# Performance work log

Hardware: AMD Instinct MI355X
Metric: run time of the kernel (lower is better)

Reference implementation:

```python
import jax, jax.numpy as jnp
import numpy as np

B, S, D, H = 2, 2048, 1024, 16
HD = D // H  # head_dim = 64


def setup_inputs() -> dict:
    key = jax.random.key(0)
    ks = jax.random.split(key, 5)
    scale = 1.0 / np.sqrt(D)
    return {
        "x": jax.random.normal(ks[0], (B, S, D), jnp.float32),
        "Wq": jax.random.normal(ks[1], (D, D), jnp.float32) * scale,
        "Wk": jax.random.normal(ks[2], (D, D), jnp.float32) * scale,
        "Wv": jax.random.normal(ks[3], (D, D), jnp.float32) * scale,
        "Wo": jax.random.normal(ks[4], (D, D), jnp.float32) * scale,
        "bo": jnp.zeros((D,), jnp.float32),
    }


def reference(x, Wq, Wk, Wv, Wo, bo):
    b, s, d = x.shape
    # torch nn.Linear: y = x @ W.T  (W stored [d_out, d_in])
    q = (x @ Wq.T).reshape(b, s, H, HD).transpose(0, 2, 1, 3)  # [b,h,s,hd]
    k = (x @ Wk.T).reshape(b, s, H, HD).transpose(0, 2, 1, 3)
    v = (x @ Wv.T).reshape(b, s, H, HD).transpose(0, 2, 1, 3)
    scores = jnp.einsum("bhqd,bhkd->bhqk", q, k) / jnp.sqrt(jnp.float32(HD))
    causal = jnp.triu(jnp.ones((s, s), dtype=bool), k=1)
    scores = jnp.where(causal[None, None], -jnp.inf, scores)
    attn = jax.nn.softmax(scores, axis=-1)
    ctx = jnp.einsum("bhqk,bhkd->bhqd", attn, v)
    ctx = ctx.transpose(0, 2, 1, 3).reshape(b, s, d)
    return ctx @ Wo.T + bo
```

## Files before the change

### kernel.cpp

```cpp
#include <hip/hip_runtime.h>

#define B_  2
#define S_  2048
#define D_  1024
#define H_  16
#define HD_ 64
#define M_  4096

typedef __attribute__((ext_vector_type(8))) short  short8;
typedef __attribute__((ext_vector_type(4))) float  floatx4;

__device__ __forceinline__ unsigned short f2bf(float f) {
  unsigned int u = __float_as_uint(f);
  u = (u + 0x7fffu + ((u >> 16) & 1u)) >> 16;
  return (unsigned short)u;
}

__device__ __forceinline__ void gl_lds16(const short* g, short* l) {
  __builtin_amdgcn_global_load_lds(
      (const __attribute__((address_space(1))) unsigned int*)g,
      (__attribute__((address_space(3))) unsigned int*)l, 16, 0, 0);
}

__global__ __launch_bounds__(256) void cast_kernel(
    const float* __restrict__ x,  const float* __restrict__ wq,
    const float* __restrict__ wk, const float* __restrict__ wv,
    const float* __restrict__ wo,
    short* __restrict__ xb,  short* __restrict__ wqb, short* __restrict__ wkb,
    short* __restrict__ wvb, short* __restrict__ wob) {
  const float* src; short* dst; int n8;
  switch (blockIdx.y) {
    case 0:  src = x;  dst = xb;  n8 = (M_ * D_) / 8; break;
    case 1:  src = wq; dst = wqb; n8 = (D_ * D_) / 8; break;
    case 2:  src = wk; dst = wkb; n8 = (D_ * D_) / 8; break;
    case 3:  src = wv; dst = wvb; n8 = (D_ * D_) / 8; break;
    default: src = wo; dst = wob; n8 = (D_ * D_) / 8; break;
  }
  int i = blockIdx.x * 256 + threadIdx.x;
  if (i >= n8) return;
  float4 a = ((const float4*)src)[2 * i];
  float4 b = ((const float4*)src)[2 * i + 1];
  short8 o;
  o[0] = (short)f2bf(a.x); o[1] = (short)f2bf(a.y);
  o[2] = (short)f2bf(a.z); o[3] = (short)f2bf(a.w);
  o[4] = (short)f2bf(b.x); o[5] = (short)f2bf(b.y);
  o[6] = (short)f2bf(b.z); o[7] = (short)f2bf(b.w);
  ((short8*)dst)[i] = o;
}

__global__ __launch_bounds__(256) void gemm_qkv(
    const short* __restrict__ xb,  const short* __restrict__ wqb,
    const short* __restrict__ wkb, const short* __restrict__ wvb,
    short* __restrict__ qo, short* __restrict__ ko, short* __restrict__ vto) {
  __shared__ alignas(16) short As[128 * 32];
  __shared__ alignas(16) short Bs[128 * 32];
  const int tid  = threadIdx.x;
  const int lane = tid & 63, wid = tid >> 6;
  const int quad = lane >> 4, l16 = lane & 15;
  const int bn = blockIdx.x, bm = blockIdx.y, z = blockIdx.z;
  const short* wsel = (z == 0) ? wqb : ((z == 1) ? wkb : wvb);
  const float scale = (z == 0) ? 0.125f * 1.44269504f : 1.0f;
  const int lrow = wid * 32 + (lane >> 2);
  const int lcol = (lane & 3) * 8;
  const short* ag0 = xb   + (bm * 128 + lrow) * D_ + lcol;
  const short* ag1 = ag0 + 16 * D_;
  const short* bg0 = wsel + (bn * 128 + lrow) * D_ + lcol;
  const short* bg1 = bg0 + 16 * D_;
  short* la0 = &As[(wid * 32) * 32];
  short* la1 = &As[(wid * 32 + 16) * 32];
  short* lb0 = &Bs[(wid * 32) * 32];
  short* lb1 = &Bs[(wid * 32 + 16) * 32];
  const int wm = (wid & 1) * 64, wn = (wid >> 1) * 64;
  floatx4 acc[4][4];
#pragma unroll
  for (int i = 0; i < 4; i++)
#pragma unroll
    for (int j = 0; j < 4; j++) acc[i][j] = (floatx4){0.f, 0.f, 0.f, 0.f};

  for (int k0 = 0; k0 < D_; k0 += 32) {
    __syncthreads();
    gl_lds16(ag0 + k0, la0);
    gl_lds16(ag1 + k0, la1);
    gl_lds16(bg0 + k0, lb0);
    gl_lds16(bg1 + k0, lb1);
    __syncthreads();
    short8 af[4], bf[4];
#pragma unroll
    for (int t = 0; t < 4; t++) af[t] = *(const short8*)&As[(wm + t * 16 + l16) * 32 + quad * 8];
#pragma unroll
    for (int t = 0; t < 4; t++) bf[t] = *(const short8*)&Bs[(wn + t * 16 + l16) * 32 + quad * 8];
#pragma unroll
    for (int tm = 0; tm < 4; tm++)
#pragma unroll
      for (int tn = 0; tn < 4; tn++)
        acc[tm][tn] = __builtin_amdgcn_mfma_f32_16x16x32_bf16(af[tm], bf[tn], acc[tm][tn], 0, 0, 0);
  }
#pragma unroll
  for (int tm = 0; tm < 4; tm++) {
#pragma unroll
    for (int tn = 0; tn < 4; tn++) {
      int n = bn * 128 + wn + tn * 16 + l16;
      int h = n >> 6, hd = n & 63;
#pragma unroll
      for (int r = 0; r < 4; r++) {
        int m = bm * 128 + wm + tm * 16 + quad * 4 + r;
        int b = m >> 11, s = m & 2047;
        unsigned short val = f2bf(acc[tm][tn][r] * scale);
        if (z == 2)
          vto[((b * H_ + h) * HD_ + hd) * S_ + s] = (short)val;
        else if (z == 1)
          ko[((b * H_ + h) * S_ + s) * HD_ + hd] = (short)val;
        else
          qo[((b * H_ + h) * S_ + s) * HD_ + hd] = (short)val;
      }
    }
  }
}

__global__ __launch_bounds__(256) void gemm_out(
    const short* __restrict__ cx, const short* __restrict__ wob,
    const float* __restrict__ bo, float* __restrict__ out) {
  __shared__ alignas(16) short As[128 * 32];
  __shared__ alignas(16) short Bs[128 * 32];
  const int tid  = threadIdx.x;
  const int lane = tid & 63, wid = tid >> 6;
  const int quad = lane >> 4, l16 = lane & 15;
  const int bn = blockIdx.x, bm = blockIdx.y;
  const int lrow = wid * 32 + (lane >> 2);
  const int lcol = (lane & 3) * 8;
  const short* ag0 = cx  + (bm * 128 + lrow) * D_ + lcol;
  const short* ag1 = ag0 + 16 * D_;
  const short* bg0 = wob + (bn * 128 + lrow) * D_ + lcol;
  const short* bg1 = bg0 + 16 * D_;
  short* la0 = &As[(wid * 32) * 32];
  short* la1 = &As[(wid * 32 + 16) * 32];
  short* lb0 = &Bs[(wid * 32) * 32];
  short* lb1 = &Bs[(wid * 32 + 16) * 32];
  const int wm = (wid & 1) * 64, wn = (wid >> 1) * 64;
  floatx4 acc[4][4];
#pragma unroll
  for (int i = 0; i < 4; i++)
#pragma unroll
    for (int j = 0; j < 4; j++) acc[i][j] = (floatx4){0.f, 0.f, 0.f, 0.f};

  for (int k0 = 0; k0 < D_; k0 += 32) {
    __syncthreads();
    gl_lds16(ag0 + k0, la0);
    gl_lds16(ag1 + k0, la1);
    gl_lds16(bg0 + k0, lb0);
    gl_lds16(bg1 + k0, lb1);
    __syncthreads();
    short8 af[4], bf[4];
#pragma unroll
    for (int t = 0; t < 4; t++) af[t] = *(const short8*)&As[(wm + t * 16 + l16) * 32 + quad * 8];
#pragma unroll
    for (int t = 0; t < 4; t++) bf[t] = *(const short8*)&Bs[(wn + t * 16 + l16) * 32 + quad * 8];
#pragma unroll
    for (int tm = 0; tm < 4; tm++)
#pragma unroll
      for (int tn = 0; tn < 4; tn++)
        acc[tm][tn] = __builtin_amdgcn_mfma_f32_16x16x32_bf16(af[tm], bf[tn], acc[tm][tn], 0, 0, 0);
  }
#pragma unroll
  for (int tn = 0; tn < 4; tn++) {
    int n = bn * 128 + wn + tn * 16 + l16;
    float bias = bo[n];
#pragma unroll
    for (int tm = 0; tm < 4; tm++) {
#pragma unroll
      for (int r = 0; r < 4; r++) {
        int m = bm * 128 + wm + tm * 16 + quad * 4 + r;
        out[m * D_ + n] = acc[tm][tn][r] + bias;
      }
    }
  }
}

__global__ __launch_bounds__(512) void attn_kernel(
    const short* __restrict__ qbuf, const short* __restrict__ kbuf,
    const short* __restrict__ vtbuf, short* __restrict__ ctx) {
  __shared__ alignas(16) short Ks[2][64][64];
  __shared__ alignas(16) short Vs[2][64][64];
  __shared__ alignas(16) short Ps[8][16][64];
  const int tid  = threadIdx.x;
  const int lane = tid & 63, wid = tid >> 6;
  const int quad = lane >> 4, l16 = lane & 15;
  const int bx = blockIdx.x, by = blockIdx.y;
  const int qt = ((by >> 4) & 1) ? bx : (15 - bx);
  const int bh = by;
  const int base = bh * (S_ * HD_);
  const int q0 = qt * 128 + wid * 16;
  const int NT = 2 * qt + 2;

  short8 qf0 = *(const short8*)(qbuf + base + (q0 + l16) * HD_ + quad * 8);
  short8 qf1 = *(const short8*)(qbuf + base + (q0 + l16) * HD_ + 32 + quad * 8);

  float lsum[4];
  floatx4 o[4];
#pragma unroll
  for (int r = 0; r < 4; r++) lsum[r] = 0.f;
#pragma unroll
  for (int nt = 0; nt < 4; nt++) o[nt] = (floatx4){0.f, 0.f, 0.f, 0.f};

  const int srow  = tid >> 3;
  const int sslot = tid & 7;
  const int swz   = ((sslot ^ (srow & 7)) << 3);
  const short* kg = kbuf  + base + srow * HD_ + sslot * 8;
  const short* vg = vtbuf + base + srow * S_  + sslot * 8;

  short8 kreg = *(const short8*)(kg);
  short8 vreg = *(const short8*)(vg);
  *(short8*)&Ks[0][srow][swz] = kreg;
  *(short8*)&Vs[0][srow][swz] = vreg;
  kreg = *(const short8*)(kg + 64 * HD_);
  vreg = *(const short8*)(vg + 64);
  __syncthreads();

  const int x16 = l16 & 7;
  for (int kt = 0; kt < NT; kt++) {
    const int b = kt & 1;
    if (kt + 1 < NT) {
      *(short8*)&Ks[b ^ 1][srow][swz] = kreg;
      *(short8*)&Vs[b ^ 1][srow][swz] = vreg;
    }
    if (kt + 2 < NT) {
      kreg = *(const short8*)(kg + (kt + 2) * 64 * HD_);
      vreg = *(const short8*)(vg + (kt + 2) * 64);
    }
    if (kt * 64 <= q0 + 15) {
      floatx4 sc[4];
#pragma unroll
      for (int ct = 0; ct < 4; ct++) {
        int row = ct * 16 + l16, rx = row & 7;
        short8 kb0 = *(const short8*)&Ks[b][row][(quad ^ rx) << 3];
        short8 kb1 = *(const short8*)&Ks[b][row][((4 + quad) ^ rx) << 3];
        floatx4 zz = (floatx4){-32.f, -32.f, -32.f, -32.f};
        zz     = __builtin_amdgcn_mfma_f32_16x16x32_bf16(qf0, kb0, zz, 0, 0, 0);
        sc[ct] = __builtin_amdgcn_mfma_f32_16x16x32_bf16(qf1, kb1, zz, 0, 0, 0);
      }
      if (kt * 64 + 63 > q0) {
#pragma unroll
        for (int ct = 0; ct < 4; ct++)
#pragma unroll
          for (int r = 0; r < 4; r++)
            if (kt * 64 + ct * 16 + l16 > q0 + quad * 4 + r) sc[ct][r] = -INFINITY;
      }
#pragma unroll
      for (int r = 0; r < 4; r++) {
        int prow = quad * 4 + r, px = prow & 7;
#pragma unroll
        for (int ct = 0; ct < 4; ct++) {
          float p = __builtin_amdgcn_exp2f(sc[ct][r]);
          lsum[r] += p;
          int cslot = ct * 2 + (l16 >> 3);
          Ps[wid][prow][((cslot ^ px) << 3) + x16] = (short)(__float_as_uint(p) >> 16);
        }
      }
#pragma unroll
      for (int ks = 0; ks < 2; ks++) {
        short8 pa = *(const short8*)&Ps[wid][l16][((ks * 4 + quad) ^ x16) << 3];
#pragma unroll
        for (int nt = 0; nt < 4; nt++) {
          int vrow = nt * 16 + l16;
          short8 vb = *(const short8*)&Vs[b][vrow][((ks * 4 + quad) ^ (vrow & 7)) << 3];
          o[nt] = __builtin_amdgcn_mfma_f32_16x16x32_bf16(pa, vb, o[nt], 0, 0, 0);
        }
      }
    }
    __syncthreads();
  }
#pragma unroll
  for (int r = 0; r < 4; r++) {
    float ls = lsum[r];
    ls += __shfl_xor(ls, 1);
    ls += __shfl_xor(ls, 2);
    ls += __shfl_xor(ls, 4);
    ls += __shfl_xor(ls, 8);
    float linv = 1.f / ls;
    int s = q0 + quad * 4 + r;
    int rowbase = ((bh >> 4) * S_ + s) * D_ + (bh & 15) * HD_;
#pragma unroll
    for (int nt = 0; nt < 4; nt++)
      ctx[rowbase + nt * 16 + l16] = (short)f2bf(o[nt][r] * linv);
  }
}

extern "C" void kernel_launch(void* const* d_in, const int* in_sizes, int n_in,
                              void* d_out, int out_size, void* d_ws, size_t ws_size,
                              hipStream_t stream) {
  const float* x  = (const float*)d_in[0];
  const float* wq = (const float*)d_in[1];
  const float* wk = (const float*)d_in[2];
  const float* wv = (const float*)d_in[3];
  const float* wo = (const float*)d_in[4];
  const float* bo = (const float*)d_in[5];
  float* out = (float*)d_out;

  char* ws = (char*)d_ws;
  short* xb  = (short*)(ws);
  short* wqb = (short*)(ws + (8u  << 20));
  short* wkb = (short*)(ws + (10u << 20));
  short* wvb = (short*)(ws + (12u << 20));
  short* wob = (short*)(ws + (14u << 20));
  short* qb  = (short*)(ws + (16u << 20));
  short* kb  = (short*)(ws + (24u << 20));
  short* cx  = (short*)(ws + (32u << 20));
  short* vtb = (short*)(ws + (40u << 20));

  cast_kernel<<<dim3(2048, 5), 256, 0, stream>>>(x, wq, wk, wv, wo, xb, wqb, wkb, wvb, wob);
  gemm_qkv   <<<dim3(8, 32, 3), 256, 0, stream>>>(xb, wqb, wkb, wvb, qb, kb, vtb);
  attn_kernel<<<dim3(16, 32),   512, 0, stream>>>(qb, kb, vtb, cx);
  gemm_out   <<<dim3(8, 32),    256, 0, stream>>>(cx, wob, bo, out);
}
```

Baseline: 179.0 us.

## Enlarge QKV GEMM tiles to 256x256 with 4-stage LDS prefetch pipeline

```diff
diff --git a/kernel.cpp b/kernel.cpp
--- a/kernel.cpp
+++ b/kernel.cpp
@@ -48,62 +48,106 @@
   ((short8*)dst)[i] = o;
 }
 
-__global__ __launch_bounds__(256) void gemm_qkv(
+__global__ __launch_bounds__(512, 1) void gemm_qkv(
     const short* __restrict__ xb,  const short* __restrict__ wqb,
     const short* __restrict__ wkb, const short* __restrict__ wvb,
     short* __restrict__ qo, short* __restrict__ ko, short* __restrict__ vto) {
-  __shared__ alignas(16) short As[128 * 32];
-  __shared__ alignas(16) short Bs[128 * 32];
+  __shared__ alignas(16) short As[4][256 * 32];
+  __shared__ alignas(16) short Bs[4][256 * 32];
   const int tid  = threadIdx.x;
   const int lane = tid & 63, wid = tid >> 6;
   const int quad = lane >> 4, l16 = lane & 15;
   const int bn = blockIdx.x, bm = blockIdx.y, z = blockIdx.z;
   const short* wsel = (z == 0) ? wqb : ((z == 1) ? wkb : wvb);
   const float scale = (z == 0) ? 0.125f * 1.44269504f : 1.0f;
-  const int lrow = wid * 32 + (lane >> 2);
-  const int lcol = (lane & 3) * 8;
-  const short* ag0 = xb   + (bm * 128 + lrow) * D_ + lcol;
-  const short* ag1 = ag0 + 16 * D_;
-  const short* bg0 = wsel + (bn * 128 + lrow) * D_ + lcol;
-  const short* bg1 = bg0 + 16 * D_;
-  short* la0 = &As[(wid * 32) * 32];
-  short* la1 = &As[(wid * 32 + 16) * 32];
-  short* lb0 = &Bs[(wid * 32) * 32];
-  short* lb1 = &Bs[(wid * 32 + 16) * 32];
-  const int wm = (wid & 1) * 64, wn = (wid >> 1) * 64;
-  floatx4 acc[4][4];
-#pragma unroll
-  for (int i = 0; i < 4; i++)
+  const int wm = (wid & 1) * 128;
+  const int wn = (wid >> 1) * 64;
+
+  const int srow = wid * 16 + (lane >> 2);
+  const int sk   = (lane & 3) * 8;
+  const short* agA = xb   + (bm * 256 + srow) * D_ + sk;
+  const short* agB = wsel + (bn * 256 + srow) * D_ + sk;
+  short* ldsA0 = &As[0][(wid * 16) * 32];
+  short* ldsB0 = &Bs[0][(wid * 16) * 32];
+
+  floatx4 acc[8][4];
+#pragma unroll
+  for (int i = 0; i < 8; i++)
 #pragma unroll
     for (int j = 0; j < 4; j++) acc[i][j] = (floatx4){0.f, 0.f, 0.f, 0.f};
 
-  for (int k0 = 0; k0 < D_; k0 += 32) {
-    __syncthreads();
-    gl_lds16(ag0 + k0, la0);
-    gl_lds16(ag1 + k0, la1);
-    gl_lds16(bg0 + k0, lb0);
-    gl_lds16(bg1 + k0, lb1);
-    __syncthreads();
-    short8 af[4], bf[4];
-#pragma unroll
-    for (int t = 0; t < 4; t++) af[t] = *(const short8*)&As[(wm + t * 16 + l16) * 32 + quad * 8];
-#pragma unroll
-    for (int t = 0; t < 4; t++) bf[t] = *(const short8*)&Bs[(wn + t * 16 + l16) * 32 + quad * 8];
+#pragma unroll
+  for (int tt = 0; tt < 3; tt++) {
+    const int kk = tt * 32;
+    gl_lds16(agA + kk,            ldsA0 + tt * (256 * 32));
+    gl_lds16(agA + 128 * D_ + kk, ldsA0 + tt * (256 * 32) + 128 * 32);
+    gl_lds16(agB + kk,            ldsB0 + tt * (256 * 32));
+    gl_lds16(agB + 128 * D_ + kk, ldsB0 + tt * (256 * 32) + 128 * 32);
+  }
+  asm volatile("s_waitcnt vmcnt(8)" ::: "memory");
+  __builtin_amdgcn_s_barrier();
+
+  for (int t = 0; t < 32; ++t) {
+    const int bq = t & 3;
+    const short* Ab = &As[bq][0];
+    const short* Bb = &Bs[bq][0];
+    const int nb = (t + 3) & 3;
+    const int kk = (t + 3) * 32;
+    const bool st = (t + 3 < 32);
+    short8 bf[4], af[4];
+#pragma unroll
+    for (int i = 0; i < 4; i++)
+      bf[i] = *(const short8*)&Bb[(wn + i * 16 + l16) * 32 + quad * 8];
+#pragma unroll
+    for (int i = 0; i < 4; i++)
+      af[i] = *(const short8*)&Ab[(wm + i * 16 + l16) * 32 + quad * 8];
+    if (st) {
+      gl_lds16(agA + kk,            ldsA0 + nb * (256 * 32));
+      gl_lds16(agA + 128 * D_ + kk, ldsA0 + nb * (256 * 32) + 128 * 32);
+    }
+    __builtin_amdgcn_s_barrier();
+    asm volatile("s_waitcnt lgkmcnt(0)" ::: "memory");
+    __builtin_amdgcn_sched_barrier(0);
+    __builtin_amdgcn_s_setprio(1);
 #pragma unroll
     for (int tm = 0; tm < 4; tm++)
 #pragma unroll
       for (int tn = 0; tn < 4; tn++)
         acc[tm][tn] = __builtin_amdgcn_mfma_f32_16x16x32_bf16(af[tm], bf[tn], acc[tm][tn], 0, 0, 0);
-  }
-#pragma unroll
-  for (int tm = 0; tm < 4; tm++) {
+    __builtin_amdgcn_s_setprio(0);
+    __builtin_amdgcn_sched_barrier(0);
+    __builtin_amdgcn_s_barrier();
+#pragma unroll
+    for (int i = 0; i < 4; i++)
+      af[i] = *(const short8*)&Ab[(wm + 64 + i * 16 + l16) * 32 + quad * 8];
+    if (st) {
+      gl_lds16(agB + kk,            ldsB0 + nb * (256 * 32));
+      gl_lds16(agB + 128 * D_ + kk, ldsB0 + nb * (256 * 32) + 128 * 32);
+    }
+    __builtin_amdgcn_s_barrier();
+    asm volatile("s_waitcnt lgkmcnt(0)" ::: "memory");
+    __builtin_amdgcn_sched_barrier(0);
+    __builtin_amdgcn_s_setprio(1);
+#pragma unroll
+    for (int tm = 0; tm < 4; tm++)
+#pragma unroll
+      for (int tn = 0; tn < 4; tn++)
+        acc[4 + tm][tn] = __builtin_amdgcn_mfma_f32_16x16x32_bf16(af[tm], bf[tn], acc[4 + tm][tn], 0, 0, 0);
+    __builtin_amdgcn_s_setprio(0);
+    __builtin_amdgcn_sched_barrier(0);
+    asm volatile("s_waitcnt vmcnt(4)" ::: "memory");
+    __builtin_amdgcn_s_barrier();
+  }
+
+#pragma unroll
+  for (int tm = 0; tm < 8; tm++) {
 #pragma unroll
     for (int tn = 0; tn < 4; tn++) {
-      int n = bn * 128 + wn + tn * 16 + l16;
+      int n = bn * 256 + wn + tn * 16 + l16;
       int h = n >> 6, hd = n & 63;
 #pragma unroll
       for (int r = 0; r < 4; r++) {
-        int m = bm * 128 + wm + tm * 16 + quad * 4 + r;
+        int m = bm * 256 + wm + tm * 16 + quad * 4 + r;
         int b = m >> 11, s = m & 2047;
         unsigned short val = f2bf(acc[tm][tn][r] * scale);
         if (z == 2)
@@ -308,7 +352,7 @@
   short* vtb = (short*)(ws + (40u << 20));
 
   cast_kernel<<<dim3(2048, 5), 256, 0, stream>>>(x, wq, wk, wv, wo, xb, wqb, wkb, wvb, wob);
-  gemm_qkv   <<<dim3(8, 32, 3), 256, 0, stream>>>(xb, wqb, wkb, wvb, qb, kb, vtb);
+  gemm_qkv   <<<dim3(4, 16, 3), 512, 0, stream>>>(xb, wqb, wkb, wvb, qb, kb, vtb);
   attn_kernel<<<dim3(16, 32),   512, 0, stream>>>(qb, kb, vtb, cx);
   gemm_out   <<<dim3(8, 32),    256, 0, stream>>>(cx, wob, bo, out);
 }
```

New measurement: 202.0 us. 1.13x slower.
